# Performance work log

Measured on AMD Instinct MI355X. Metric: run time of the kernel, lower is better.

The kernel has to match this reference:

```python
import jax, jax.numpy as jnp
import numpy as np

N_NODES = 50000
N_EDGES = 800000
IN_FEATS = 128
HID = 64
HEADS = 3
NUM_CLASSES = 8
ATTN_SLOPE = 0.2   # DGL GATConv leaky_relu slope on attention logits
ACT_SLOPE = 0.01   # nn.LeakyReLU default


def setup_inputs() -> dict:
    key = jax.random.key(0)
    ks = jax.random.split(key, 40)
    inp = {}
    inp["x"] = jax.random.normal(ks[0], (N_NODES, IN_FEATS), dtype=jnp.float32)
    inp["src"] = jax.random.randint(ks[1], (N_EDGES,), 0, N_NODES)
    inp["dst"] = jax.random.randint(ks[2], (N_EDGES,), 0, N_NODES)
    dims_in = [IN_FEATS, HID, HID, HID, HID]
    i = 3
    for l, din in enumerate(dims_in, start=1):
        inp[f"W{l}"] = jax.random.normal(ks[i], (din, HEADS * HID), dtype=jnp.float32) / np.float32(np.sqrt(din)); i += 1
        inp[f"b{l}"] = jnp.zeros((HEADS * HID,), dtype=jnp.float32)
        inp[f"al{l}"] = jax.random.normal(ks[i], (HEADS, HID), dtype=jnp.float32) * 0.1; i += 1
        inp[f"ar{l}"] = jax.random.normal(ks[i], (HEADS, HID), dtype=jnp.float32) * 0.1; i += 1
    inp["Wo"] = jax.random.normal(ks[i], (HID, NUM_CLASSES), dtype=jnp.float32) / np.float32(np.sqrt(HID)); i += 1
    inp["bo"] = jnp.zeros((NUM_CLASSES,), dtype=jnp.float32)
    return inp


def _gatconv(h, W, b, al, ar, src, dst):
    # h: [N, din] -> feat: [N, H, F]
    feat = (h @ W).reshape(N_NODES, HEADS, HID)
    el = jnp.einsum('nhf,hf->nh', feat, al)   # [N, H]
    er = jnp.einsum('nhf,hf->nh', feat, ar)   # [N, H]
    e = jax.nn.leaky_relu(el[src] + er[dst], ATTN_SLOPE)        # [E, H]
    # numerically-stable edge softmax segmented by destination node
    m = jax.ops.segment_max(e, dst, num_segments=N_NODES)      # [N, H]
    ex = jnp.exp(e - m[dst])                                   # [E, H]
    denom = jax.ops.segment_sum(ex, dst, num_segments=N_NODES)  # [N, H]
    alpha = ex / denom[dst]                                    # [E, H]
    msg = alpha[:, :, None] * feat[src]                        # [E, H, F]
    out = jax.ops.segment_sum(msg, dst, num_segments=N_NODES)  # [N, H, F]
    return out + b.reshape(HEADS, HID)


def reference(x, src, dst,
              W1, b1, al1, ar1,
              W2, b2, al2, ar2,
              W3, b3, al3, ar3,
              W4, b4, al4, ar4,
              W5, b5, al5, ar5,
              Wo, bo):
    layers = [(W1, b1, al1, ar1), (W2, b2, al2, ar2), (W3, b3, al3, ar3),
              (W4, b4, al4, ar4), (W5, b5, al5, ar5)]
    h = x
    for (W, b, al, ar) in layers:
        h = jax.nn.leaky_relu(_gatconv(h, W, b, al, ar, src, dst), ACT_SLOPE)
        h = h.mean(axis=1)  # mean over heads -> [N, F]
    return h @ Wo + bo      # [N, num_classes]
```

## Files before the change

kernel.cpp:

```cpp
#include <hip/hip_runtime.h>
#include <hip/hip_fp16.h>
#include <cstdint>

#define N_NODES 50000
#define N_EDGES 800000
#define IN_FEATS 128
#define HID 64
#define HEADS 3
#define NUM_CLASSES 8
#define ATTN_SLOPE 0.2f
#define ACT_SLOPE 0.01f

typedef _Float16 half8 __attribute__((ext_vector_type(8)));
typedef float f32x4 __attribute__((ext_vector_type(4)));

__device__ __forceinline__ float lrelu(float x, float s) { return x > 0.f ? x : s * x; }

__global__ void k_deg(const int* __restrict__ dst, int* __restrict__ deg, int E) {
    int i = blockIdx.x * blockDim.x + threadIdx.x;
    if (i < E) atomicAdd(&deg[dst[i]], 1);
}

__global__ __launch_bounds__(256) void k_scan1(const int* __restrict__ deg, int* __restrict__ off,
                                               int* __restrict__ bsum, int n) {
    __shared__ int wtot[4];
    int tid = threadIdx.x;
    int lane = tid & 63, wid = tid >> 6;
    int base = blockIdx.x * 2048 + tid * 8;
    int v[8];
    if (base + 8 <= n) {
        int4 a = *(const int4*)&deg[base];
        int4 b = *(const int4*)&deg[base + 4];
        v[0] = a.x; v[1] = a.y; v[2] = a.z; v[3] = a.w;
        v[4] = b.x; v[5] = b.y; v[6] = b.z; v[7] = b.w;
    } else {
#pragma unroll
        for (int j = 0; j < 8; ++j) v[j] = (base + j < n) ? deg[base + j] : 0;
    }
    int s[8];
    s[0] = v[0];
#pragma unroll
    for (int j = 1; j < 8; ++j) s[j] = s[j - 1] + v[j];
    int t = s[7];
    int incl = t;
    for (int o = 1; o < 64; o <<= 1) {
        int u = __shfl_up(incl, o);
        if (lane >= o) incl += u;
    }
    int excl = incl - t;
    if (lane == 63) wtot[wid] = incl;
    __syncthreads();
    int wprefix = 0;
    for (int w = 0; w < wid; ++w) wprefix += wtot[w];
    int base_off = wprefix + excl;
#pragma unroll
    for (int j = 0; j < 8; ++j)
        if (base + j < n) off[base + j] = base_off + s[j] - v[j];
    if (tid == 0) bsum[blockIdx.x] = wtot[0] + wtot[1] + wtot[2] + wtot[3];
}

__global__ __launch_bounds__(64) void k_scan2(int* __restrict__ bsum, int nb) {
    int tid = threadIdx.x;
    int v = (tid < nb) ? bsum[tid] : 0;
    int incl = v;
    for (int o = 1; o < 64; o <<= 1) {
        int u = __shfl_up(incl, o);
        if (tid >= o) incl += u;
    }
    if (tid < nb) bsum[tid] = incl - v;
}

__global__ __launch_bounds__(256) void k_scan3(int* __restrict__ off, const int* __restrict__ bsum,
                                               int n, int E) {
    int i = blockIdx.x * blockDim.x + threadIdx.x;
    if (i < n) off[i] += bsum[i >> 11];
    if (i == 0) off[n] = E;
}

__global__ void k_fill(const int* __restrict__ src, const int* __restrict__ dst,
                       const int* __restrict__ off, int* __restrict__ cur,
                       int* __restrict__ ssrc, int E) {
    int i = blockIdx.x * blockDim.x + threadIdx.x;
    if (i < E) {
        int d = dst[i];
        int p = atomicAdd(&cur[d], 1);
        ssrc[off[d] + p] = src[i];
    }
}

__global__ __launch_bounds__(256) void k_xcast(const float* __restrict__ x, _Float16* __restrict__ xh, int n8) {
    int i = blockIdx.x * blockDim.x + threadIdx.x;
    if (i < n8) {
        float4 a = *(const float4*)&x[i * 8];
        float4 b = *(const float4*)&x[i * 8 + 4];
        _Float16 v[8] = {(_Float16)a.x, (_Float16)a.y, (_Float16)a.z, (_Float16)a.w,
                         (_Float16)b.x, (_Float16)b.y, (_Float16)b.z, (_Float16)b.w};
        *(uint4*)&xh[i * 8] = *(uint4*)v;
    }
}

__global__ __launch_bounds__(256) void k_wcast(const float* __restrict__ W1, const float* __restrict__ W2,
                                               const float* __restrict__ W3, const float* __restrict__ W4,
                                               const float* __restrict__ W5, _Float16* __restrict__ Wt) {
    int i = blockIdx.x * blockDim.x + threadIdx.x;
    if (i >= 24576 + 4 * 12288) return;
    const float* W; int din; int idx; _Float16* out;
    if (i < 24576) { W = W1; din = 128; idx = i; out = Wt; }
    else {
        int j = i - 24576; int l = j / 12288; idx = j % 12288;
        W = (l == 0) ? W2 : (l == 1) ? W3 : (l == 2) ? W4 : W5;
        din = 64;
        out = Wt + 24576 + l * 12288;
    }
    int col = idx / din, k = idx % din;
    out[idx] = (_Float16)W[k * 192 + col];
}

__global__ __launch_bounds__(256) void k_gemm(const _Float16* __restrict__ h, const _Float16* __restrict__ Wt,
                                              const float* __restrict__ al, const float* __restrict__ ar,
                                              _Float16* __restrict__ feat,
                                              float* __restrict__ el, float* __restrict__ er,
                                              int N, int din) {
    __shared__ __align__(16) _Float16 Hl[128 * 136];
    __shared__ __align__(16) _Float16 Wl[64 * 136];
    const int K = din;
    const int LD = K + 8;
    const int KC = K >> 3;
    int tid = threadIdx.x;
    int row0 = blockIdx.x * 128;
    int head = blockIdx.y;
    int c0 = head * 64;

    for (int i = tid; i < 64 * KC; i += 256) {
        int col = i / KC, c8 = i % KC;
        *(uint4*)&Wl[col * LD + c8 * 8] = *(const uint4*)&Wt[(size_t)(c0 + col) * K + c8 * 8];
    }
    for (int i = tid; i < 128 * KC; i += 256) {
        int r = i / KC, c8 = i % KC;
        int row = row0 + r;
        uint4 v = make_uint4(0, 0, 0, 0);
        if (row < N) v = *(const uint4*)&h[(size_t)row * K + c8 * 8];
        *(uint4*)&Hl[r * LD + c8 * 8] = v;
    }
    __syncthreads();

    int wid = tid >> 6, lane = tid & 63;
    int l15 = lane & 15;
    int koff = (lane >> 4) * 8;
    int wr0 = wid * 32;

    f32x4 acc[2][4] = {};
    int nkb = K >> 5;
    for (int kb = 0; kb < nkb; ++kb) {
        int kbase = kb * 32 + koff;
        half8 a0 = *(half8*)&Hl[(wr0 + l15) * LD + kbase];
        half8 a1 = *(half8*)&Hl[(wr0 + 16 + l15) * LD + kbase];
        half8 b0 = *(half8*)&Wl[(l15) * LD + kbase];
        half8 b1 = *(half8*)&Wl[(16 + l15) * LD + kbase];
        half8 b2 = *(half8*)&Wl[(32 + l15) * LD + kbase];
        half8 b3 = *(half8*)&Wl[(48 + l15) * LD + kbase];
        acc[0][0] = __builtin_amdgcn_mfma_f32_16x16x32_f16(a0, b0, acc[0][0], 0, 0, 0);
        acc[0][1] = __builtin_amdgcn_mfma_f32_16x16x32_f16(a0, b1, acc[0][1], 0, 0, 0);
        acc[0][2] = __builtin_amdgcn_mfma_f32_16x16x32_f16(a0, b2, acc[0][2], 0, 0, 0);
        acc[0][3] = __builtin_amdgcn_mfma_f32_16x16x32_f16(a0, b3, acc[0][3], 0, 0, 0);
        acc[1][0] = __builtin_amdgcn_mfma_f32_16x16x32_f16(a1, b0, acc[1][0], 0, 0, 0);
        acc[1][1] = __builtin_amdgcn_mfma_f32_16x16x32_f16(a1, b1, acc[1][1], 0, 0, 0);
        acc[1][2] = __builtin_amdgcn_mfma_f32_16x16x32_f16(a1, b2, acc[1][2], 0, 0, 0);
        acc[1][3] = __builtin_amdgcn_mfma_f32_16x16x32_f16(a1, b3, acc[1][3], 0, 0, 0);
    }

    float alv[4], arv[4];
#pragma unroll
    for (int ct = 0; ct < 4; ++ct) {
        alv[ct] = al[c0 + ct * 16 + l15];
        arv[ct] = ar[c0 + ct * 16 + l15];
    }

#pragma unroll
    for (int rt = 0; rt < 2; ++rt) {
#pragma unroll
        for (int r = 0; r < 4; ++r) {
            int row = row0 + wr0 + rt * 16 + (lane >> 4) * 4 + r;
            bool ok = (row < N);
            float c0v = acc[rt][0][r], c1v = acc[rt][1][r], c2v = acc[rt][2][r], c3v = acc[rt][3][r];
            if (ok) {
                size_t base = (size_t)row * 192 + c0;
                feat[base + l15]      = (_Float16)c0v;
                feat[base + 16 + l15] = (_Float16)c1v;
                feat[base + 32 + l15] = (_Float16)c2v;
                feat[base + 48 + l15] = (_Float16)c3v;
            }
            float pl = c0v * alv[0] + c1v * alv[1] + c2v * alv[2] + c3v * alv[3];
            float pr = c0v * arv[0] + c1v * arv[1] + c2v * arv[2] + c3v * arv[3];
            for (int o = 1; o < 16; o <<= 1) {
                pl += __shfl_xor(pl, o);
                pr += __shfl_xor(pr, o);
            }
            if (ok && l15 == 0) {
                el[row * HEADS + head] = pl;
                er[row * HEADS + head] = pr;
            }
        }
    }
}

__global__ __launch_bounds__(256) void k_agg(const int* __restrict__ off, const int* __restrict__ ssrc,
                                             const float* __restrict__ el, const float* __restrict__ er,
                                             const __half* __restrict__ feat, const float* __restrict__ b,
                                             __half* __restrict__ hout, int N) {
    __shared__ float4 ebuf[4][64];
    int wib = threadIdx.x >> 6;
    int wid = (blockIdx.x * blockDim.x + threadIdx.x) >> 6;
    int lane = threadIdx.x & 63;
    if (wid >= N) return;
    int start = off[wid], end = off[wid + 1];
    int cnt = end - start;
    float er0 = er[wid * HEADS + 0];
    float er1 = er[wid * HEADS + 1];
    float er2 = er[wid * HEADS + 2];
    float acc0 = 0.f, acc1 = 0.f, acc2 = 0.f;
    float den0 = 0.f, den1 = 0.f, den2 = 0.f;

    if (cnt <= 64) {
        int s0 = 0;
        float ea = -3.4e38f, eb = -3.4e38f, ec = -3.4e38f;
        if (lane < cnt) {
            s0 = ssrc[start + lane];
            ea = lrelu(el[s0 * HEADS + 0] + er0, ATTN_SLOPE);
            eb = lrelu(el[s0 * HEADS + 1] + er1, ATTN_SLOPE);
            ec = lrelu(el[s0 * HEADS + 2] + er2, ATTN_SLOPE);
        }
        float ma = ea, mb = eb, mc = ec;
        for (int o = 32; o > 0; o >>= 1) {
            ma = fmaxf(ma, __shfl_xor(ma, o));
            mb = fmaxf(mb, __shfl_xor(mb, o));
            mc = fmaxf(mc, __shfl_xor(mc, o));
        }
        float xa = (lane < cnt) ? __expf(ea - ma) : 0.f;
        float xb = (lane < cnt) ? __expf(eb - mb) : 0.f;
        float xc = (lane < cnt) ? __expf(ec - mc) : 0.f;
        float da = xa, db = xb, dc = xc;
        for (int o = 32; o > 0; o >>= 1) {
            da += __shfl_xor(da, o);
            db += __shfl_xor(db, o);
            dc += __shfl_xor(dc, o);
        }
        den0 = da; den1 = db; den2 = dc;
        ebuf[wib][lane] = make_float4(__int_as_float(s0), xa, xb, xc);
        int t = 0;
        for (; t + 4 <= cnt; t += 4) {
            float4 v0 = ebuf[wib][t + 0];
            float4 v1 = ebuf[wib][t + 1];
            float4 v2 = ebuf[wib][t + 2];
            float4 v3 = ebuf[wib][t + 3];
            const __half* f0 = feat + (size_t)__float_as_int(v0.x) * 192 + lane;
            const __half* f1 = feat + (size_t)__float_as_int(v1.x) * 192 + lane;
            const __half* f2 = feat + (size_t)__float_as_int(v2.x) * 192 + lane;
            const __half* f3 = feat + (size_t)__float_as_int(v3.x) * 192 + lane;
            float p00 = __half2float(f0[0]), p01 = __half2float(f0[64]), p02 = __half2float(f0[128]);
            float p10 = __half2float(f1[0]), p11 = __half2float(f1[64]), p12 = __half2float(f1[128]);
            float p20 = __half2float(f2[0]), p21 = __half2float(f2[64]), p22 = __half2float(f2[128]);
            float p30 = __half2float(f3[0]), p31 = __half2float(f3[64]), p32 = __half2float(f3[128]);
            acc0 += v0.y * p00; acc1 += v0.z * p01; acc2 += v0.w * p02;
            acc0 += v1.y * p10; acc1 += v1.z * p11; acc2 += v1.w * p12;
            acc0 += v2.y * p20; acc1 += v2.z * p21; acc2 += v2.w * p22;
            acc0 += v3.y * p30; acc1 += v3.z * p31; acc2 += v3.w * p32;
        }
        for (; t < cnt; ++t) {
            float4 v = ebuf[wib][t];
            const __half* fr = feat + (size_t)__float_as_int(v.x) * 192 + lane;
            acc0 += v.y * __half2float(fr[0]);
            acc1 += v.z * __half2float(fr[64]);
            acc2 += v.w * __half2float(fr[128]);
        }
    } else {
        float ma = -3.4e38f, mb = -3.4e38f, mc = -3.4e38f;
        for (int j = start + lane; j < end; j += 64) {
            int s = ssrc[j];
            ma = fmaxf(ma, lrelu(el[s * HEADS + 0] + er0, ATTN_SLOPE));
            mb = fmaxf(mb, lrelu(el[s * HEADS + 1] + er1, ATTN_SLOPE));
            mc = fmaxf(mc, lrelu(el[s * HEADS + 2] + er2, ATTN_SLOPE));
        }
        for (int o = 32; o > 0; o >>= 1) {
            ma = fmaxf(ma, __shfl_xor(ma, o));
            mb = fmaxf(mb, __shfl_xor(mb, o));
            mc = fmaxf(mc, __shfl_xor(mc, o));
        }
        float da = 0.f, db = 0.f, dc = 0.f;
        for (int j0 = start; j0 < end; j0 += 64) {
            int jj = j0 + lane;
            int s0 = 0;
            float xa = 0.f, xb = 0.f, xc = 0.f;
            if (jj < end) {
                s0 = ssrc[jj];
                xa = __expf(lrelu(el[s0 * HEADS + 0] + er0, ATTN_SLOPE) - ma);
                xb = __expf(lrelu(el[s0 * HEADS + 1] + er1, ATTN_SLOPE) - mb);
                xc = __expf(lrelu(el[s0 * HEADS + 2] + er2, ATTN_SLOPE) - mc);
            }
            da += xa; db += xb; dc += xc;
            ebuf[wib][lane] = make_float4(__int_as_float(s0), xa, xb, xc);
            int c = min(64, end - j0);
            int t = 0;
            for (; t + 4 <= c; t += 4) {
                float4 v0 = ebuf[wib][t + 0];
                float4 v1 = ebuf[wib][t + 1];
                float4 v2 = ebuf[wib][t + 2];
                float4 v3 = ebuf[wib][t + 3];
                const __half* f0 = feat + (size_t)__float_as_int(v0.x) * 192 + lane;
                const __half* f1 = feat + (size_t)__float_as_int(v1.x) * 192 + lane;
                const __half* f2 = feat + (size_t)__float_as_int(v2.x) * 192 + lane;
                const __half* f3 = feat + (size_t)__float_as_int(v3.x) * 192 + lane;
                float p00 = __half2float(f0[0]), p01 = __half2float(f0[64]), p02 = __half2float(f0[128]);
                float p10 = __half2float(f1[0]), p11 = __half2float(f1[64]), p12 = __half2float(f1[128]);
                float p20 = __half2float(f2[0]), p21 = __half2float(f2[64]), p22 = __half2float(f2[128]);
                float p30 = __half2float(f3[0]), p31 = __half2float(f3[64]), p32 = __half2float(f3[128]);
                acc0 += v0.y * p00; acc1 += v0.z * p01; acc2 += v0.w * p02;
                acc0 += v1.y * p10; acc1 += v1.z * p11; acc2 += v1.w * p12;
                acc0 += v2.y * p20; acc1 += v2.z * p21; acc2 += v2.w * p22;
                acc0 += v3.y * p30; acc1 += v3.z * p31; acc2 += v3.w * p32;
            }
            for (; t < c; ++t) {
                float4 v = ebuf[wib][t];
                const __half* fr = feat + (size_t)__float_as_int(v.x) * 192 + lane;
                acc0 += v.y * __half2float(fr[0]);
                acc1 += v.z * __half2float(fr[64]);
                acc2 += v.w * __half2float(fr[128]);
            }
        }
        for (int o = 32; o > 0; o >>= 1) {
            da += __shfl_xor(da, o);
            db += __shfl_xor(db, o);
            dc += __shfl_xor(dc, o);
        }
        den0 = da; den1 = db; den2 = dc;
    }

    float v0 = (cnt > 0) ? acc0 / den0 : 0.f;
    float v1 = (cnt > 0) ? acc1 / den1 : 0.f;
    float v2 = (cnt > 0) ? acc2 / den2 : 0.f;
    float hsum = lrelu(v0 + b[lane], ACT_SLOPE)
               + lrelu(v1 + b[64 + lane], ACT_SLOPE)
               + lrelu(v2 + b[128 + lane], ACT_SLOPE);
    hout[wid * 64 + lane] = __float2half(hsum * (1.f / 3.f));
}

__global__ __launch_bounds__(256) void k_out(const __half* __restrict__ h, const float* __restrict__ Wo,
                                             const float* __restrict__ bo, float* __restrict__ out, int N) {
    __shared__ float Hl[32][65];
    __shared__ float Wl[64 * 8];
    int tid = threadIdx.x;
    int n0 = blockIdx.x * 32;
    for (int i = tid; i < 32 * 64; i += 256) {
        int r = i >> 6, k = i & 63;
        Hl[r][k] = (n0 + r < N) ? __half2float(h[(n0 + r) * 64 + k]) : 0.f;
    }
    for (int i = tid; i < 512; i += 256) Wl[i] = Wo[i];
    __syncthreads();
    int r = tid >> 3, c = tid & 7;
    float acc = 0.f;
    for (int k = 0; k < 64; ++k) acc += Hl[r][k] * Wl[k * 8 + c];
    int row = n0 + r;
    if (row < N) out[row * 8 + c] = acc + bo[c];
}

extern "C" void kernel_launch(void* const* d_in, const int* in_sizes, int n_in,
                              void* d_out, int out_size, void* d_ws, size_t ws_size,
                              hipStream_t stream) {
    const float* x  = (const float*)d_in[0];
    const int* src  = (const int*)d_in[1];
    const int* dst  = (const int*)d_in[2];
    const float *W[5], *b[5], *al[5], *ar[5];
    for (int l = 0; l < 5; ++l) {
        W[l]  = (const float*)d_in[3 + l * 4];
        b[l]  = (const float*)d_in[4 + l * 4];
        al[l] = (const float*)d_in[5 + l * 4];
        ar[l] = (const float*)d_in[6 + l * 4];
    }
    const float* Wo = (const float*)d_in[23];
    const float* bo = (const float*)d_in[24];
    float* out = (float*)d_out;

    char* ws = (char*)d_ws;
    auto alloc = [&](size_t bytes) {
        char* p = ws;
        ws += (bytes + 255) & ~size_t(255);
        return p;
    };
    _Float16* feat = (_Float16*)alloc(sizeof(_Float16) * (size_t)N_NODES * 192);
    float* el      = (float*)alloc(sizeof(float) * (size_t)N_NODES * HEADS);
    float* er      = (float*)alloc(sizeof(float) * (size_t)N_NODES * HEADS);
    _Float16* xh   = (_Float16*)alloc(sizeof(_Float16) * (size_t)N_NODES * IN_FEATS);
    _Float16* h0   = (_Float16*)alloc(sizeof(_Float16) * (size_t)N_NODES * 64);
    _Float16* h1   = (_Float16*)alloc(sizeof(_Float16) * (size_t)N_NODES * 64);
    _Float16* wt   = (_Float16*)alloc(sizeof(_Float16) * (24576 + 4 * 12288));
    int* deg    = (int*)alloc(sizeof(int) * N_NODES);
    int* off    = (int*)alloc(sizeof(int) * (N_NODES + 1));
    int* cur    = (int*)alloc(sizeof(int) * N_NODES);
    int* ssrc   = (int*)alloc(sizeof(int) * N_EDGES);
    int* bsum   = (int*)alloc(sizeof(int) * 64);

    const int NB = (N_NODES + 2047) / 2048;
    (void)hipMemsetAsync(deg, 0, sizeof(int) * N_NODES, stream);
    (void)hipMemsetAsync(cur, 0, sizeof(int) * N_NODES, stream);
    k_deg<<<(N_EDGES + 255) / 256, 256, 0, stream>>>(dst, deg, N_EDGES);
    k_scan1<<<NB, 256, 0, stream>>>(deg, off, bsum, N_NODES);
    k_scan2<<<1, 64, 0, stream>>>(bsum, NB);
    k_scan3<<<(N_NODES + 255) / 256, 256, 0, stream>>>(off, bsum, N_NODES, N_EDGES);
    k_fill<<<(N_EDGES + 255) / 256, 256, 0, stream>>>(src, dst, off, cur, ssrc, N_EDGES);
    k_xcast<<<(N_NODES * IN_FEATS / 8 + 255) / 256, 256, 0, stream>>>(x, xh, N_NODES * IN_FEATS / 8);
    k_wcast<<<(24576 + 4 * 12288 + 255) / 256, 256, 0, stream>>>(W[0], W[1], W[2], W[3], W[4], wt);

    const _Float16* hin = xh;
    _Float16* hbuf[2] = {h0, h1};
    const _Float16* wts[5] = {wt, wt + 24576, wt + 24576 + 12288, wt + 24576 + 2 * 12288, wt + 24576 + 3 * 12288};
    int din = IN_FEATS;
    for (int l = 0; l < 5; ++l) {
        dim3 ggrid((N_NODES + 127) / 128, HEADS);
        k_gemm<<<ggrid, 256, 0, stream>>>(hin, wts[l], al[l], ar[l], feat, el, er, N_NODES, din);
        _Float16* hn = hbuf[l & 1];
        k_agg<<<(N_NODES * 64 + 255) / 256, 256, 0, stream>>>(off, ssrc, el, er,
                                                              (const __half*)feat, b[l],
                                                              (__half*)hn, N_NODES);
        hin = hn;
        din = HID;
    }
    k_out<<<(N_NODES + 31) / 32, 256, 0, stream>>>((const __half*)hin, Wo, bo, out, N_NODES);
}
```

Measured before the change: 537.0 us.

## Split GAT aggregation per head into separate waves plus combine kernel

Each wave in the aggregation kernel now handles one node and one head, so each node has three waves. It writes a per-head partial result (activated, scaled by 1/3) to a scratch buffer, and a new combine kernel sums the three heads in fp16. The goal is to cut per-wave register and latency pressure, increase parallelism and memory-level parallelism on the gathers, and group blocks by head for better cache locality. In exchange, edge indices and attention logits are read three times, there is an extra scratch write and read pass and an extra kernel launch per layer, and summing in fp16 adds a little rounding error.

```diff
diff --git a/kernel.cpp b/kernel.cpp
--- a/kernel.cpp
+++ b/kernel.cpp
@@ -204,144 +204,134 @@
     }
 }
 
-__global__ __launch_bounds__(256) void k_agg(const int* __restrict__ off, const int* __restrict__ ssrc,
-                                             const float* __restrict__ el, const float* __restrict__ er,
-                                             const __half* __restrict__ feat, const float* __restrict__ b,
-                                             __half* __restrict__ hout, int N) {
-    __shared__ float4 ebuf[4][64];
+__global__ __launch_bounds__(256) void k_aggh(const int* __restrict__ off, const int* __restrict__ ssrc,
+                                              const float* __restrict__ el, const float* __restrict__ er,
+                                              const __half* __restrict__ feat, const float* __restrict__ bias,
+                                              __half* __restrict__ pout, int N) {
+    __shared__ float2 ebuf[4][64];
+    int s = blockIdx.x & 7, q = blockIdx.x >> 3;
+    int head, idx, ch;
+    if (s < 3)      { head = 0; idx = s;     ch = 3; }
+    else if (s < 6) { head = 1; idx = s - 3; ch = 3; }
+    else            { head = 2; idx = s - 6; ch = 2; }
     int wib = threadIdx.x >> 6;
-    int wid = (blockIdx.x * blockDim.x + threadIdx.x) >> 6;
+    int n = (q * ch + idx) * 4 + wib;
+    if (n >= N) return;
     int lane = threadIdx.x & 63;
-    if (wid >= N) return;
-    int start = off[wid], end = off[wid + 1];
+    int start = off[n], end = off[n + 1];
     int cnt = end - start;
-    float er0 = er[wid * HEADS + 0];
-    float er1 = er[wid * HEADS + 1];
-    float er2 = er[wid * HEADS + 2];
-    float acc0 = 0.f, acc1 = 0.f, acc2 = 0.f;
-    float den0 = 0.f, den1 = 0.f, den2 = 0.f;
+    float erh = er[n * HEADS + head];
+    const __half* fb = feat + head * 64 + lane;
+    float acc = 0.f, den = 0.f;
 
     if (cnt <= 64) {
         int s0 = 0;
-        float ea = -3.4e38f, eb = -3.4e38f, ec = -3.4e38f;
+        float e = -3.4e38f;
         if (lane < cnt) {
             s0 = ssrc[start + lane];
-            ea = lrelu(el[s0 * HEADS + 0] + er0, ATTN_SLOPE);
-            eb = lrelu(el[s0 * HEADS + 1] + er1, ATTN_SLOPE);
-            ec = lrelu(el[s0 * HEADS + 2] + er2, ATTN_SLOPE);
-        }
-        float ma = ea, mb = eb, mc = ec;
-        for (int o = 32; o > 0; o >>= 1) {
-            ma = fmaxf(ma, __shfl_xor(ma, o));
-            mb = fmaxf(mb, __shfl_xor(mb, o));
-            mc = fmaxf(mc, __shfl_xor(mc, o));
-        }
-        float xa = (lane < cnt) ? __expf(ea - ma) : 0.f;
-        float xb = (lane < cnt) ? __expf(eb - mb) : 0.f;
-        float xc = (lane < cnt) ? __expf(ec - mc) : 0.f;
-        float da = xa, db = xb, dc = xc;
-        for (int o = 32; o > 0; o >>= 1) {
-            da += __shfl_xor(da, o);
-            db += __shfl_xor(db, o);
-            dc += __shfl_xor(dc, o);
-        }
-        den0 = da; den1 = db; den2 = dc;
-        ebuf[wib][lane] = make_float4(__int_as_float(s0), xa, xb, xc);
+            e = lrelu(el[s0 * HEADS + head] + erh, ATTN_SLOPE);
+        }
+        float m = e;
+        for (int o = 32; o > 0; o >>= 1) m = fmaxf(m, __shfl_xor(m, o));
+        float x = (lane < cnt) ? __expf(e - m) : 0.f;
+        float d = x;
+        for (int o = 32; o > 0; o >>= 1) d += __shfl_xor(d, o);
+        den = d;
+        ebuf[wib][lane] = make_float2(__int_as_float(s0), x);
         int t = 0;
-        for (; t + 4 <= cnt; t += 4) {
-            float4 v0 = ebuf[wib][t + 0];
-            float4 v1 = ebuf[wib][t + 1];
-            float4 v2 = ebuf[wib][t + 2];
-            float4 v3 = ebuf[wib][t + 3];
-            const __half* f0 = feat + (size_t)__float_as_int(v0.x) * 192 + lane;
-            const __half* f1 = feat + (size_t)__float_as_int(v1.x) * 192 + lane;
-            const __half* f2 = feat + (size_t)__float_as_int(v2.x) * 192 + lane;
-            const __half* f3 = feat + (size_t)__float_as_int(v3.x) * 192 + lane;
-            float p00 = __half2float(f0[0]), p01 = __half2float(f0[64]), p02 = __half2float(f0[128]);
-            float p10 = __half2float(f1[0]), p11 = __half2float(f1[64]), p12 = __half2float(f1[128]);
-            float p20 = __half2float(f2[0]), p21 = __half2float(f2[64]), p22 = __half2float(f2[128]);
-            float p30 = __half2float(f3[0]), p31 = __half2float(f3[64]), p32 = __half2float(f3[128]);
-            acc0 += v0.y * p00; acc1 += v0.z * p01; acc2 += v0.w * p02;
-            acc0 += v1.y * p10; acc1 += v1.z * p11; acc2 += v1.w * p12;
-            acc0 += v2.y * p20; acc1 += v2.z * p21; acc2 += v2.w * p22;
-            acc0 += v3.y * p30; acc1 += v3.z * p31; acc2 += v3.w * p32;
+        for (; t + 8 <= cnt; t += 8) {
+            float2 v0 = ebuf[wib][t + 0];
+            float2 v1 = ebuf[wib][t + 1];
+            float2 v2 = ebuf[wib][t + 2];
+            float2 v3 = ebuf[wib][t + 3];
+            float2 v4 = ebuf[wib][t + 4];
+            float2 v5 = ebuf[wib][t + 5];
+            float2 v6 = ebuf[wib][t + 6];
+            float2 v7 = ebuf[wib][t + 7];
+            float p0 = __half2float(fb[(size_t)__float_as_int(v0.x) * 192]);
+            float p1 = __half2float(fb[(size_t)__float_as_int(v1.x) * 192]);
+            float p2 = __half2float(fb[(size_t)__float_as_int(v2.x) * 192]);
+            float p3 = __half2float(fb[(size_t)__float_as_int(v3.x) * 192]);
+            float p4 = __half2float(fb[(size_t)__float_as_int(v4.x) * 192]);
+            float p5 = __half2float(fb[(size_t)__float_as_int(v5.x) * 192]);
+            float p6 = __half2float(fb[(size_t)__float_as_int(v6.x) * 192]);
+            float p7 = __half2float(fb[(size_t)__float_as_int(v7.x) * 192]);
+            acc += v0.y * p0 + v1.y * p1 + v2.y * p2 + v3.y * p3
+                 + v4.y * p4 + v5.y * p5 + v6.y * p6 + v7.y * p7;
         }
         for (; t < cnt; ++t) {
-            float4 v = ebuf[wib][t];
-            const __half* fr = feat + (size_t)__float_as_int(v.x) * 192 + lane;
-            acc0 += v.y * __half2float(fr[0]);
-            acc1 += v.z * __half2float(fr[64]);
-            acc2 += v.w * __half2float(fr[128]);
+            float2 v = ebuf[wib][t];
+            acc += v.y * __half2float(fb[(size_t)__float_as_int(v.x) * 192]);
         }
     } else {
-        float ma = -3.4e38f, mb = -3.4e38f, mc = -3.4e38f;
+        float m = -3.4e38f;
         for (int j = start + lane; j < end; j += 64) {
-            int s = ssrc[j];
-            ma = fmaxf(ma, lrelu(el[s * HEADS + 0] + er0, ATTN_SLOPE));
-            mb = fmaxf(mb, lrelu(el[s * HEADS + 1] + er1, ATTN_SLOPE));
-            mc = fmaxf(mc, lrelu(el[s * HEADS + 2] + er2, ATTN_SLOPE));
-        }
-        for (int o = 32; o > 0; o >>= 1) {
-            ma = fmaxf(ma, __shfl_xor(ma, o));
-            mb = fmaxf(mb, __shfl_xor(mb, o));
-            mc = fmaxf(mc, __shfl_xor(mc, o));
-        }
-        float da = 0.f, db = 0.f, dc = 0.f;
+            int sj = ssrc[j];
+            m = fmaxf(m, lrelu(el[sj * HEADS + head] + erh, ATTN_SLOPE));
+        }
+        for (int o = 32; o > 0; o >>= 1) m = fmaxf(m, __shfl_xor(m, o));
+        float d = 0.f;
         for (int j0 = start; j0 < end; j0 += 64) {
             int jj = j0 + lane;
             int s0 = 0;
-            float xa = 0.f, xb = 0.f, xc = 0.f;
+            float x = 0.f;
             if (jj < end) {
                 s0 = ssrc[jj];
-                xa = __expf(lrelu(el[s0 * HEADS + 0] + er0, ATTN_SLOPE) - ma);
-                xb = __expf(lrelu(el[s0 * HEADS + 1] + er1, ATTN_SLOPE) - mb);
-                xc = __expf(lrelu(el[s0 * HEADS + 2] + er2, ATTN_SLOPE) - mc);
-            }
-            da += xa; db += xb; dc += xc;
-            ebuf[wib][lane] = make_float4(__int_as_float(s0), xa, xb, xc);
+                x = __expf(lrelu(el[s0 * HEADS + head] + erh, ATTN_SLOPE) - m);
+            }
+            d += x;
+            ebuf[wib][lane] = make_float2(__int_as_float(s0), x);
             int c = min(64, end - j0);
             int t = 0;
-            for (; t + 4 <= c; t += 4) {
-                float4 v0 = ebuf[wib][t + 0];
-                float4 v1 = ebuf[wib][t + 1];
-                float4 v2 = ebuf[wib][t + 2];
-                float4 v3 = ebuf[wib][t + 3];
-                const __half* f0 = feat + (size_t)__float_as_int(v0.x) * 192 + lane;
-                const __half* f1 = feat + (size_t)__float_as_int(v1.x) * 192 + lane;
-                const __half* f2 = feat + (size_t)__float_as_int(v2.x) * 192 + lane;
-                const __half* f3 = feat + (size_t)__float_as_int(v3.x) * 192 + lane;
-                float p00 = __half2float(f0[0]), p01 = __half2float(f0[64]), p02 = __half2float(f0[128]);
-                float p10 = __half2float(f1[0]), p11 = __half2float(f1[64]), p12 = __half2float(f1[128]);
-                float p20 = __half2float(f2[0]), p21 = __half2float(f2[64]), p22 = __half2float(f2[128]);
-                float p30 = __half2float(f3[0]), p31 = __half2float(f3[64]), p32 = __half2float(f3[128]);
-                acc0 += v0.y * p00; acc1 += v0.z * p01; acc2 += v0.w * p02;
-                acc0 += v1.y * p10; acc1 += v1.z * p11; acc2 += v1.w * p12;
-                acc0 += v2.y * p20; acc1 += v2.z * p21; acc2 += v2.w * p22;
-                acc0 += v3.y * p30; acc1 += v3.z * p31; acc2 += v3.w * p32;
+            for (; t + 8 <= c; t += 8) {
+                float2 v0 = ebuf[wib][t + 0];
+                float2 v1 = ebuf[wib][t + 1];
+                float2 v2 = ebuf[wib][t + 2];
+                float2 v3 = ebuf[wib][t + 3];
+                float2 v4 = ebuf[wib][t + 4];
+                float2 v5 = ebuf[wib][t + 5];
+                float2 v6 = ebuf[wib][t + 6];
+                float2 v7 = ebuf[wib][t + 7];
+                float p0 = __half2float(fb[(size_t)__float_as_int(v0.x) * 192]);
+                float p1 = __half2float(fb[(size_t)__float_as_int(v1.x) * 192]);
+                float p2 = __half2float(fb[(size_t)__float_as_int(v2.x) * 192]);
+                float p3 = __half2float(fb[(size_t)__float_as_int(v3.x) * 192]);
+                float p4 = __half2float(fb[(size_t)__float_as_int(v4.x) * 192]);
+                float p5 = __half2float(fb[(size_t)__float_as_int(v5.x) * 192]);
+                float p6 = __half2float(fb[(size_t)__float_as_int(v6.x) * 192]);
+                float p7 = __half2float(fb[(size_t)__float_as_int(v7.x) * 192]);
+                acc += v0.y * p0 + v1.y * p1 + v2.y * p2 + v3.y * p3
+                     + v4.y * p4 + v5.y * p5 + v6.y * p6 + v7.y * p7;
             }
             for (; t < c; ++t) {
-                float4 v = ebuf[wib][t];
-                const __half* fr = feat + (size_t)__float_as_int(v.x) * 192 + lane;
-                acc0 += v.y * __half2float(fr[0]);
-                acc1 += v.z * __half2float(fr[64]);
-                acc2 += v.w * __half2float(fr[128]);
-            }
-        }
-        for (int o = 32; o > 0; o >>= 1) {
-            da += __shfl_xor(da, o);
-            db += __shfl_xor(db, o);
-            dc += __shfl_xor(dc, o);
-        }
-        den0 = da; den1 = db; den2 = dc;
-    }
-
-    float v0 = (cnt > 0) ? acc0 / den0 : 0.f;
-    float v1 = (cnt > 0) ? acc1 / den1 : 0.f;
-    float v2 = (cnt > 0) ? acc2 / den2 : 0.f;
-    float hsum = lrelu(v0 + b[lane], ACT_SLOPE)
-               + lrelu(v1 + b[64 + lane], ACT_SLOPE)
-               + lrelu(v2 + b[128 + lane], ACT_SLOPE);
-    hout[wid * 64 + lane] = __float2half(hsum * (1.f / 3.f));
+                float2 v = ebuf[wib][t];
+                acc += v.y * __half2float(fb[(size_t)__float_as_int(v.x) * 192]);
+            }
+        }
+        for (int o = 32; o > 0; o >>= 1) d += __shfl_xor(d, o);
+        den = d;
+    }
+
+    float vout = (cnt > 0) ? acc / den : 0.f;
+    float po = lrelu(vout + bias[head * 64 + lane], ACT_SLOPE) * (1.f / 3.f);
+    pout[((size_t)head * N + n) * 64 + lane] = __float2half(po);
+}
+
+__global__ __launch_bounds__(256) void k_comb(const __half* __restrict__ P, __half* __restrict__ hout, int n8) {
+    int i = blockIdx.x * blockDim.x + threadIdx.x;
+    if (i >= n8) return;
+    const size_t NPH = (size_t)N_NODES * 64;
+    uint4 a = *(const uint4*)&P[(size_t)i * 8];
+    uint4 b = *(const uint4*)&P[NPH + (size_t)i * 8];
+    uint4 c = *(const uint4*)&P[2 * NPH + (size_t)i * 8];
+    __half2* ah = (__half2*)&a;
+    __half2* bh = (__half2*)&b;
+    __half2* ch = (__half2*)&c;
+    uint4 r;
+    __half2* rh = (__half2*)&r;
+#pragma unroll
+    for (int k = 0; k < 4; ++k) rh[k] = __hadd2(__hadd2(ah[k], bh[k]), ch[k]);
+    *(uint4*)&hout[(size_t)i * 8] = r;
 }
 
 __global__ __launch_bounds__(256) void k_out(const __half* __restrict__ h, const float* __restrict__ Wo,
@@ -392,6 +382,7 @@
     _Float16* xh   = (_Float16*)alloc(sizeof(_Float16) * (size_t)N_NODES * IN_FEATS);
     _Float16* h0   = (_Float16*)alloc(sizeof(_Float16) * (size_t)N_NODES * 64);
     _Float16* h1   = (_Float16*)alloc(sizeof(_Float16) * (size_t)N_NODES * 64);
+    _Float16* part = (_Float16*)alloc(sizeof(_Float16) * (size_t)HEADS * N_NODES * 64);
     _Float16* wt   = (_Float16*)alloc(sizeof(_Float16) * (24576 + 4 * 12288));
     int* deg    = (int*)alloc(sizeof(int) * N_NODES);
     int* off    = (int*)alloc(sizeof(int) * (N_NODES + 1));
@@ -410,6 +401,9 @@
     k_xcast<<<(N_NODES * IN_FEATS / 8 + 255) / 256, 256, 0, stream>>>(x, xh, N_NODES * IN_FEATS / 8);
     k_wcast<<<(24576 + 4 * 12288 + 255) / 256, 256, 0, stream>>>(W[0], W[1], W[2], W[3], W[4], wt);
 
+    const int AGG_BLOCKS = 6250 * 8;
+    const int COMB_N8 = N_NODES * 64 / 8;
+
     const _Float16* hin = xh;
     _Float16* hbuf[2] = {h0, h1};
     const _Float16* wts[5] = {wt, wt + 24576, wt + 24576 + 12288, wt + 24576 + 2 * 12288, wt + 24576 + 3 * 12288};
@@ -418,9 +412,10 @@
         dim3 ggrid((N_NODES + 127) / 128, HEADS);
         k_gemm<<<ggrid, 256, 0, stream>>>(hin, wts[l], al[l], ar[l], feat, el, er, N_NODES, din);
         _Float16* hn = hbuf[l & 1];
-        k_agg<<<(N_NODES * 64 + 255) / 256, 256, 0, stream>>>(off, ssrc, el, er,
-                                                              (const __half*)feat, b[l],
-                                                              (__half*)hn, N_NODES);
+        k_aggh<<<AGG_BLOCKS, 256, 0, stream>>>(off, ssrc, el, er,
+                                               (const __half*)feat, b[l],
+                                               (__half*)part, N_NODES);
+        k_comb<<<(COMB_N8 + 255) / 256, 256, 0, stream>>>((const __half*)part, (__half*)hn, COMB_N8);
         hin = hn;
         din = HID;
     }
```

New measurement: 852.8 us. +58.8%, slower.
